# Optimization experiments

Measured on AMD Instinct MI355X. Metric: run time of the kernel, lower is better.

The kernel has to match this reference:

```python
import jax, jax.numpy as jnp
import numpy as np

EPS = 1e-6
SCALE = 1.0
GRID_HEIGHT = 4.0
GRID_RES_Y = 1.0


def _perspective(mat, vec):
    # mat [3,4], vec [...,3] -> (points [...,2], flag [...,3])
    homog = jnp.einsum('ij,...j->...i', mat[:, :3], vec) + mat[:, 3]
    pos = homog[..., 2:3] > 0
    flag = jnp.concatenate([pos, pos, jnp.ones_like(pos)], axis=-1).astype(homog.dtype)
    homog = homog * flag  # zero x,y behind camera; z kept (flag[...,-1]=True)
    return homog[..., :2] / homog[..., 2:3], flag


def _fisheye(pts, k, D, flag):
    cx, cy, fx, fy = k[0, 2], k[1, 2], k[0, 0], k[1, 1]
    x = (pts[..., 0] - cx) / fx
    y = (pts[..., 1] - cy) / fy
    r = jnp.sqrt(x * x + y * y)
    th = jnp.arctan(r)
    t2 = th * th
    rad = th * (1 + D[0] * t2 + D[1] * t2 ** 2 + D[2] * t2 ** 3 + D[5] * t2 ** 4) / r
    xd = x * rad * fx + cx
    yd = y * rad * fy + cy
    return jnp.stack([xd, yd], axis=-1) * flag[..., :2]


def _pinhole(pts, k, D, flag):
    cx, cy, fx, fy = k[0, 2], k[1, 2], k[0, 0], k[1, 1]
    x = (pts[..., 0] - cx) / fx
    y = (pts[..., 1] - cy) / fy
    k1, k2, k3, p1, p2 = D[0], D[1], D[2], D[3], D[4]
    r2 = x * x + y * y
    poly = 1 + k1 * r2 + k2 * r2 * r2 + k3 * r2 * r2 * r2
    xd = x * poly + (2 * p1 * x * y + p2 * (r2 + 2 * x * x))
    yd = y * poly + (p1 * (r2 + 2 * y * y) + 2 * p2 * x * y)
    return jnp.stack([xd * fx + cx, yd * fy + cy], axis=-1) * flag[..., :2]


def _bilinear(img, coords):
    # torch F.grid_sample(align_corners=True, padding_mode='border'); img [C,H,W], coords [...,2] in [-1,1]
    C, H, W = img.shape
    x = jnp.clip((coords[..., 0] + 1) * 0.5 * (W - 1), 0.0, W - 1)
    y = jnp.clip((coords[..., 1] + 1) * 0.5 * (H - 1), 0.0, H - 1)
    x0 = jnp.floor(x)
    y0 = jnp.floor(y)
    wx = x - x0
    wy = y - y0
    x0i = x0.astype(jnp.int32)
    y0i = y0.astype(jnp.int32)
    x1i = jnp.minimum(x0i + 1, W - 1)
    y1i = jnp.minimum(y0i + 1, H - 1)
    flat = img.reshape(C, H * W)

    def g(yi, xi):
        return jnp.take(flat, (yi * W + xi).reshape(-1), axis=1).reshape((C,) + coords.shape[:-1])

    v00 = g(y0i, x0i)
    v01 = g(y0i, x1i)
    v10 = g(y1i, x0i)
    v11 = g(y1i, x1i)
    return v00 * (1 - wx) * (1 - wy) + v01 * wx * (1 - wy) + v10 * (1 - wx) * wy + v11 * wx * wy


def _per_image(feature, k, imu2c, post_rot, post_tran, undist, corner):
    C, Hf, Wf = feature.shape
    calib = k @ imu2c                                  # [3,4]
    pts, flag = _perspective(calib, corner)            # pts [Ny,Zd,Xd,2]
    pts = jnp.where(undist[-1] == 1,
                    _fisheye(pts, k, undist, flag),
                    _pinhole(pts, k, undist, flag))
    pts = jnp.einsum('ij,...j->...i', post_rot[:2, :2], pts) + post_tran[:2]
    nc = jnp.clip(2.0 * (pts / SCALE) - 1.0, -1.0, 1.0)  # [Ny,Zd,Xd,2]
    s0, s1 = slice(None, -1), slice(1, None)
    # 8 voxel corners -> [8, Ny-1, D, Wd, 2]
    corners8 = jnp.stack([nc[a, b, c] for a in (s0, s1) for b in (s0, s1) for c in (s0, s1)], axis=0)
    left = corners8[..., 0].min(0)
    right = corners8[..., 0].max(0)
    top = corners8[..., 1].min(0)
    bot = corners8[..., 1].max(0)
    Nh, D, Wd = left.shape
    bbox = jnp.stack([left, top, right, bot], axis=-1).reshape(Nh, D * Wd, 4)
    area = (bbox[..., 2] - bbox[..., 0]) * (bbox[..., 3] - bbox[..., 1]) * Hf * Wf * 0.25 + EPS  # [Nh,P]
    integ = jnp.cumsum(jnp.cumsum(feature, axis=-1), axis=-2)  # integral image [C,Hf,Wf]
    tl = _bilinear(integ, bbox[..., 0:2])
    br = _bilinear(integ, bbox[..., 2:4])
    tr = _bilinear(integ, jnp.stack([bbox[..., 2], bbox[..., 1]], axis=-1))
    bl = _bilinear(integ, jnp.stack([bbox[..., 0], bbox[..., 3]], axis=-1))
    vox = (tl + br - tr - bl) / area * (area > EPS)    # [C,Nh,P]
    return vox.reshape(C * Nh, D, Wd)                  # neck == '2d'


def _forward(features, ks, imu2cs, post_rots, post_trans, undists, grid):
    ys = -jnp.arange(0.0, GRID_HEIGHT, GRID_RES_Y) + GRID_HEIGHT / 2.0
    y_corners = jnp.stack([jnp.zeros_like(ys), ys, jnp.zeros_like(ys)], axis=-1)  # [Ny,3]
    corners = grid[:, None] + y_corners[None, :, None, None, :]                   # [B,Ny,Zd,Xd,3]
    per_cam = jax.vmap(_per_image, in_axes=(0, 0, 0, 0, 0, 0, None))

    def per_batch(f, k, m, pr, pt, ud, c):
        # drop_idx = [] -> all cameras kept; max over cameras
        return per_cam(f, k, m, pr, pt, ud, c).max(axis=0)

    return jax.vmap(per_batch)(features, ks, imu2cs, post_rots, post_trans, undists, corners)


def setup_inputs():
    key = jax.random.key(0)
    B, N, C, Hf, Wf = 1, 6, 64, 64, 176
    Zd = Xd = 129
    kf, ku = jax.random.split(key, 2)
    features = jax.random.normal(kf, (B, N, C, Hf, Wf), jnp.float32)
    # intrinsics (realistic pinhole values keep the projection numerically sane)
    K = np.zeros((B, N, 3, 3), np.float32)
    K[..., 0, 0] = 600.0
    K[..., 1, 1] = 600.0
    K[..., 0, 2] = 704.0
    K[..., 1, 2] = 256.0
    K[..., 2, 2] = 1.0
    ks = jnp.asarray(K)
    # extrinsics: per-camera yaw + small translation
    m = np.zeros((B, N, 3, 4), np.float32)
    for i in range(N):
        th = 0.25 * (i - 2.5)
        R = np.array([[np.cos(th), 0.0, np.sin(th)],
                      [0.0, 1.0, 0.0],
                      [-np.sin(th), 0.0, np.cos(th)]], np.float32)
        m[:, i, :, :3] = R
        m[:, i, :, 3] = np.array([0.1 * i, -1.5, 0.2], np.float32)
    imu2cs = jnp.asarray(m)
    pr = np.zeros((B, N, 3, 3), np.float32)
    pr[..., 0, 0] = 1.0 / 1408.0
    pr[..., 1, 1] = 1.0 / 512.0
    pr[..., 2, 2] = 1.0
    post_rots = jnp.asarray(pr)
    post_trans = jnp.zeros((B, N, 3), jnp.float32)
    und = 0.01 * np.array(jax.random.normal(ku, (B, N, 7)), np.float32)
    und[..., 6] = 0.0
    und[:, :3, 6] = 1.0  # first 3 cameras fisheye, rest pinhole
    undists = jnp.asarray(und)
    x = np.linspace(-40.0, 40.0, Xd, dtype=np.float32)
    z = np.linspace(3.0, 80.0, Zd, dtype=np.float32)
    zz, xx = np.meshgrid(z, x, indexing='ij')
    g = np.stack([xx, np.zeros_like(xx), zz], axis=-1)[None]  # [1,Zd,Xd,3]
    grid = jnp.asarray(np.broadcast_to(g, (B, Zd, Xd, 3)).copy())
    return {"features": features, "ks": ks, "imu2cs": imu2cs, "post_rots": post_rots,
            "post_trans": post_trans, "undists": undists, "grid": grid}


def reference(features, ks, imu2cs, post_rots, post_trans, undists, grid):
    return _forward(features, ks, imu2cs, post_rots, post_trans, undists, grid)
```

## Files before the change

### kernel.cpp

```cpp
#include <hip/hip_runtime.h>
#include <math.h>

#define NCAM 6
#define C_CH 64
#define HF   64
#define WF   176
#define GDIM 129
#define NY   4
#define NH   3
#define DD   128
#define WDIM 128
#define NP   (DD*WDIM)

#define ROWB (WF*C_CH*4)
#define COLB (C_CH*4)
#define IMGB ((size_t)HF*WF*C_CH*4)


__device__ __forceinline__ float bcf(int x) {
    return __builtin_bit_cast(float, x);
}

__global__ __launch_bounds__(256) void k_rowcum(const float* __restrict__ feat,
                                                float* __restrict__ rowsum)
{
    __shared__ float T[WF * 65];
    __shared__ float S[4][C_CH];
    __shared__ float OFF[4][C_CH];
    const int h   = blockIdx.x;
    const int n   = blockIdx.y;
    const int tid = threadIdx.x;

    for (int idx = tid; idx < C_CH * WF; idx += 256) {
        const int cc = idx / WF;
        const int w  = idx % WF;
        T[w*65 + cc] = feat[((size_t)(n*C_CH + cc)*HF + h)*WF + w];
    }
    __syncthreads();
    {
        const int cc = tid & 63, seg = tid >> 6;
        const int w0 = seg * 44;
        float run = 0.0f;
        #pragma unroll
        for (int i = 0; i < 44; ++i) {
            run += T[(w0 + i)*65 + cc];
            T[(w0 + i)*65 + cc] = run;
        }
        S[seg][cc] = run;
    }
    __syncthreads();
    {
        const int cc = tid & 63, seg = tid >> 6;
        float off = 0.0f;
        #pragma unroll
        for (int s = 0; s < 3; ++s)
            if (s < seg) off += S[s][cc];
        OFF[seg][cc] = off;
    }
    __syncthreads();
    float* outp = rowsum + (size_t)(n*HF + h) * (WF * C_CH);
    for (int idx = tid; idx < WF * C_CH; idx += 256) {
        const int w  = idx >> 6;
        const int cc = idx & 63;
        outp[idx] = T[w*65 + cc] + OFF[w/44][cc];
    }
}

__global__ __launch_bounds__(256) void k_colcum(float* __restrict__ integ)
{
    __shared__ float tA[4][C_CH];
    const int x  = blockIdx.x;
    const int n  = blockIdx.y;
    const int c  = threadIdx.x & 63;
    const int hq = threadIdx.x >> 6;

    float* base = integ + (size_t)n*HF*WF*C_CH + (size_t)x * C_CH + c;
    float e[16];
    #pragma unroll
    for (int i = 0; i < 16; ++i)
        e[i] = base[(size_t)(hq*16 + i) * (WF*C_CH)];
    #pragma unroll
    for (int i = 1; i < 16; ++i)
        e[i] += e[i-1];
    tA[hq][c] = e[15];
    __syncthreads();
    float off = 0.0f;
    #pragma unroll
    for (int s = 0; s < 3; ++s)
        if (s < hq) off += tA[s][c];
    #pragma unroll
    for (int i = 0; i < 16; ++i)
        base[(size_t)(hq*16 + i) * (WF*C_CH)] = e[i] + off;
}

__global__ void k_boxproj(const float* __restrict__ ks,
                          const float* __restrict__ imu2cs,
                          const float* __restrict__ post_rots,
                          const float* __restrict__ post_trans,
                          const float* __restrict__ undists,
                          const float* __restrict__ grid,
                          int4* __restrict__ bp)
{
    const int idx = blockIdx.x * blockDim.x + threadIdx.x;
    if (idx >= NCAM * NH * NP) return;
    const int vox = idx / NCAM;
    const int n   = idx - vox * NCAM;
    const int nh  = vox / NP;
    const int p   = vox - nh * NP;
    const int d   = p / WDIM;
    const int wd  = p - d * WDIM;

    const float* k  = ks         + n * 9;
    const float* m  = imu2cs     + n * 12;
    const float* pr = post_rots  + n * 9;
    const float* pt = post_trans + n * 3;
    const float* D  = undists    + n * 7;

    float cal[12];
    #pragma unroll
    for (int i = 0; i < 3; ++i)
        #pragma unroll
        for (int j = 0; j < 4; ++j)
            cal[i*4+j] = k[i*3+0]*m[0*4+j] + k[i*3+1]*m[1*4+j] + k[i*3+2]*m[2*4+j];

    const float fx = k[0], fy = k[4], cx = k[2], cy = k[5];
    const bool fish = (D[6] == 1.0f);
    const float D0 = D[0], D1 = D[1], D2 = D[2], D3 = D[3], D4 = D[4], D5 = D[5];

    float left = 1e30f, right = -1e30f, top = 1e30f, bot = -1e30f;
    #pragma unroll
    for (int a = 0; a < 2; ++a) {
        const float vy = 2.0f - (float)(nh + a);
        #pragma unroll
        for (int b = 0; b < 2; ++b) {
            #pragma unroll
            for (int cc = 0; cc < 2; ++cc) {
                const int gz = d + b, gx = wd + cc;
                const float vx = grid[(gz*GDIM + gx)*3 + 0];
                const float vz = grid[(gz*GDIM + gx)*3 + 2];

                const float hx = cal[0]*vx + cal[1]*vy + cal[2]*vz  + cal[3];
                const float hy = cal[4]*vx + cal[5]*vy + cal[6]*vz  + cal[7];
                const float hz = cal[8]*vx + cal[9]*vy + cal[10]*vz + cal[11];

                const float fl = (hz > 0.0f) ? 1.0f : 0.0f;
                const float px = (hx * fl) / hz;
                const float py = (hy * fl) / hz;

                const float x = (px - cx) / fx;
                const float y = (py - cy) / fy;

                float xd, yd;
                if (fish) {
                    const float rr = sqrtf(x*x + y*y);
                    const float th = atanf(rr);
                    const float t2 = th * th;
                    const float t4 = t2 * t2;
                    const float rad = th * (1.0f + D0*t2 + D1*t4 + D2*(t2*t4) + D5*(t4*t4)) / rr;
                    xd = x * rad * fx + cx;
                    yd = y * rad * fy + cy;
                } else {
                    const float r2 = x*x + y*y;
                    const float poly = 1.0f + D0*r2 + D1*r2*r2 + D2*r2*r2*r2;
                    const float xdd = x*poly + (2.0f*D3*x*y + D4*(r2 + 2.0f*x*x));
                    const float ydd = y*poly + (D3*(r2 + 2.0f*y*y) + 2.0f*D4*x*y);
                    xd = xdd * fx + cx;
                    yd = ydd * fy + cy;
                }
                xd *= fl; yd *= fl;

                const float qx = pr[0]*xd + pr[1]*yd + pt[0];
                const float qy = pr[3]*xd + pr[4]*yd + pt[1];
                const float ncx = fminf(fmaxf(2.0f*qx - 1.0f, -1.0f), 1.0f);
                const float ncy = fminf(fmaxf(2.0f*qy - 1.0f, -1.0f), 1.0f);

                left  = fminf(left,  ncx);  right = fmaxf(right, ncx);
                top   = fminf(top,   ncy);  bot   = fmaxf(bot,   ncy);
            }
        }
    }

    const float area = (right - left) * (bot - top) * (float)HF * (float)WF * 0.25f + 1e-6f;

    const float xLp = fminf(fmaxf((left  + 1.0f) * 0.5f * (float)(WF-1), 0.0f), (float)(WF-1));
    const float xRp = fminf(fmaxf((right + 1.0f) * 0.5f * (float)(WF-1), 0.0f), (float)(WF-1));
    const float yTp = fminf(fmaxf((top   + 1.0f) * 0.5f * (float)(HF-1), 0.0f), (float)(HF-1));
    const float yBp = fminf(fmaxf((bot   + 1.0f) * 0.5f * (float)(HF-1), 0.0f), (float)(HF-1));
    const float xL0 = floorf(xLp), xR0 = floorf(xRp), yT0 = floorf(yTp), yB0 = floorf(yBp);

    const int pyx = (int)yT0 | ((int)yB0 << 8) | ((int)xL0 << 16) | ((int)xR0 << 24);

    int4 o0, o1;
    o0.x = pyx;
    o0.y = __builtin_bit_cast(int, xLp - xL0);
    o0.z = __builtin_bit_cast(int, xRp - xR0);
    o0.w = __builtin_bit_cast(int, yTp - yT0);
    o1.x = __builtin_bit_cast(int, yBp - yB0);
    o1.y = __builtin_bit_cast(int, area);
    o1.z = 0; o1.w = 0;
    bp[(size_t)idx*2 + 0] = o0;
    bp[(size_t)idx*2 + 1] = o1;
}

__global__ __launch_bounds__(256, 4) void k_sample(const float* __restrict__ integ,
                                                   const int* __restrict__ bpi,
                                                   float* __restrict__ out)
{
    __shared__ float sm[64][65];
    const int nh   = blockIdx.y;
    const int p0   = blockIdx.x * 64;
    const int tid  = threadIdx.x;
    const int wave = __builtin_amdgcn_readfirstlane(tid >> 6);
    const int c    = tid & 63;
    const int pl   = (c < 48) ? c : (c - 48);

    const int* bpw = bpi + (size_t)(nh*NP + p0 + wave*16) * 48;

    int vpc = bpw[pl];
    #pragma unroll 1
    for (int j = 0; j < 16; ++j) {
        int vpn = vpc;
        if (j < 15) vpn = bpw[(j + 1) * 48 + pl];

        float t[6][16];
        float wxl[6], wxr[6], wyt[6], wyb[6], ar[6];
        #pragma unroll
        for (int cam = 0; cam < 6; ++cam) {
            const int f0 = __builtin_amdgcn_readlane(vpc, cam*8 + 0);
            wxl[cam] = bcf(__builtin_amdgcn_readlane(vpc, cam*8 + 1));
            wxr[cam] = bcf(__builtin_amdgcn_readlane(vpc, cam*8 + 2));
            wyt[cam] = bcf(__builtin_amdgcn_readlane(vpc, cam*8 + 3));
            wyb[cam] = bcf(__builtin_amdgcn_readlane(vpc, cam*8 + 4));
            ar[cam]  = bcf(__builtin_amdgcn_readlane(vpc, cam*8 + 5));
            const int yT = f0 & 255, yB = (f0 >> 8) & 255;
            const int xL = (f0 >> 16) & 255, xR = (f0 >> 24) & 255;
            const int r0 = yT * ROWB, r2 = yB * ROWB;
            const int c0 = xL * COLB, c2 = xR * COLB;
            const char* b = (const char*)integ + (size_t)cam * IMGB;
            #pragma unroll
            for (int rr = 0; rr < 4; ++rr) {
                const int ro = ((rr < 2) ? r0 : r2) + ((rr & 1) ? ROWB : 0);
                #pragma unroll
                for (int cc2 = 0; cc2 < 4; ++cc2) {
                    const int co = ((cc2 < 2) ? c0 : c2) + ((cc2 & 1) ? COLB : 0);
                    t[cam][rr*4 + cc2] = ((const float*)(b + (size_t)(ro + co)))[c];
                }
            }
        }

        float vmax = -3.402823466e38f;
        #pragma unroll
        for (int cam = 0; cam < 6; ++cam) {
            const float A0 = fmaf(wxl[cam], t[cam][1]  - t[cam][0],  t[cam][0]);
            const float B0 = fmaf(wxr[cam], t[cam][3]  - t[cam][2],  t[cam][2]);
            const float A1 = fmaf(wxl[cam], t[cam][5]  - t[cam][4],  t[cam][4]);
            const float B1 = fmaf(wxr[cam], t[cam][7]  - t[cam][6],  t[cam][6]);
            const float A2 = fmaf(wxl[cam], t[cam][9]  - t[cam][8],  t[cam][8]);
            const float B2 = fmaf(wxr[cam], t[cam][11] - t[cam][10], t[cam][10]);
            const float A3 = fmaf(wxl[cam], t[cam][13] - t[cam][12], t[cam][12]);
            const float B3 = fmaf(wxr[cam], t[cam][15] - t[cam][14], t[cam][14]);
            const float d0 = A0 - B0, d1 = A1 - B1;
            const float e0 = B2 - A2, e1 = B3 - A3;
            const float s = fmaf(wyt[cam], d1 - d0, d0) + fmaf(wyb[cam], e1 - e0, e0);
            float v = s * __builtin_amdgcn_rcpf(ar[cam]);
            v = (ar[cam] > 1e-6f) ? v : 0.0f;
            vmax = fmaxf(vmax, v);
        }
        sm[wave*16 + j][c] = vmax;
        vpc = vpn;
    }
    __syncthreads();
    #pragma unroll
    for (int it = 0; it < 16; ++it) {
        const int idx = it*256 + tid;
        const int jj = idx & 63;
        const int cc = idx >> 6;
        out[(size_t)(cc*NH + nh)*NP + p0 + jj] = sm[jj][cc];
    }
}

extern "C" void kernel_launch(void* const* d_in, const int* in_sizes, int n_in,
                              void* d_out, int out_size, void* d_ws, size_t ws_size,
                              hipStream_t stream)
{
    const float* feats      = (const float*)d_in[0];
    const float* ks         = (const float*)d_in[1];
    const float* imu2cs     = (const float*)d_in[2];
    const float* post_rots  = (const float*)d_in[3];
    const float* post_trans = (const float*)d_in[4];
    const float* undists    = (const float*)d_in[5];
    const float* grid       = (const float*)d_in[6];
    float* out = (float*)d_out;

    char* ws = (char*)d_ws;
    size_t off = 0;
    float* integ = (float*)(ws + off);
    off += (size_t)NCAM * IMGB + 65536;
    off = (off + 255) & ~(size_t)255;
    int4* bp = (int4*)(ws + off);
    off += (size_t)NCAM * NH * NP * 32 + 256;
    (void)ws_size; (void)in_sizes; (void)n_in; (void)out_size;

    dim3 g1(HF, NCAM);
    k_rowcum<<<g1, 256, 0, stream>>>(feats, integ);

    dim3 g2(WF, NCAM);
    k_colcum<<<g2, 256, 0, stream>>>(integ);

    dim3 g3((NCAM*NH*NP + 255)/256);
    k_boxproj<<<g3, 256, 0, stream>>>(ks, imu2cs, post_rots, post_trans, undists, grid, bp);

    dim3 g4(NP/64, NH);
    k_sample<<<g4, 256, 0, stream>>>(integ, (const int*)bp, out);
}
```

Baseline: 152.1 us.

## Shrink sample tiles, pair cameras to cut registers, add XCD-aware block mapping

The sampling kernel now processes 32 points per block instead of 64 and handles cameras in pairs instead of loading all six cameras' 96 corner values at once. This lowers register pressure so the launch bound can rise to 6 blocks per SIMD. A 1D grid is remapped so consecutive tiles of the same height slice land on the same XCD, which is meant to improve L2 locality of the integral images. The projection kernel swaps IEEE divides for hardware reciprocals, which slightly changes numerics, and pairing cameras exposes less memory-level parallelism per wave.

```diff
diff --git a/kernel.cpp b/kernel.cpp
--- a/kernel.cpp
+++ b/kernel.cpp
@@ -124,6 +124,7 @@
             cal[i*4+j] = k[i*3+0]*m[0*4+j] + k[i*3+1]*m[1*4+j] + k[i*3+2]*m[2*4+j];
 
     const float fx = k[0], fy = k[4], cx = k[2], cy = k[5];
+    const float rfx = 1.0f / fx, rfy = 1.0f / fy;
     const bool fish = (D[6] == 1.0f);
     const float D0 = D[0], D1 = D[1], D2 = D[2], D3 = D[3], D4 = D[4], D5 = D[5];
 
@@ -144,11 +145,12 @@
                 const float hz = cal[8]*vx + cal[9]*vy + cal[10]*vz + cal[11];
 
                 const float fl = (hz > 0.0f) ? 1.0f : 0.0f;
-                const float px = (hx * fl) / hz;
-                const float py = (hy * fl) / hz;
-
-                const float x = (px - cx) / fx;
-                const float y = (py - cy) / fy;
+                const float rhz = __builtin_amdgcn_rcpf(hz);
+                const float px = (hx * fl) * rhz;
+                const float py = (hy * fl) * rhz;
+
+                const float x = (px - cx) * rfx;
+                const float y = (py - cy) * rfy;
 
                 float xd, yd;
                 if (fish) {
@@ -156,7 +158,8 @@
                     const float th = atanf(rr);
                     const float t2 = th * th;
                     const float t4 = t2 * t2;
-                    const float rad = th * (1.0f + D0*t2 + D1*t4 + D2*(t2*t4) + D5*(t4*t4)) / rr;
+                    const float rad = th * (1.0f + D0*t2 + D1*t4 + D2*(t2*t4) + D5*(t4*t4))
+                                      * __builtin_amdgcn_rcpf(rr);
                     xd = x * rad * fx + cx;
                     yd = y * rad * fy + cy;
                 } else {
@@ -202,79 +205,123 @@
     bp[(size_t)idx*2 + 1] = o1;
 }
 
-__global__ __launch_bounds__(256, 4) void k_sample(const float* __restrict__ integ,
+__global__ __launch_bounds__(256, 6) void k_sample(const float* __restrict__ integ,
                                                    const int* __restrict__ bpi,
                                                    float* __restrict__ out)
 {
-    __shared__ float sm[64][65];
-    const int nh   = blockIdx.y;
-    const int p0   = blockIdx.x * 64;
+    __shared__ float sm[32][65];
+    const int bx   = blockIdx.x;
+    const int xcd  = bx & 7;
+    const int slot = bx >> 3;
+    const int gt   = xcd * 192 + slot;
+    const int nh   = gt >> 9;
+    const int p0   = (gt & 511) * 32;
     const int tid  = threadIdx.x;
     const int wave = __builtin_amdgcn_readfirstlane(tid >> 6);
     const int c    = tid & 63;
     const int pl   = (c < 48) ? c : (c - 48);
 
-    const int* bpw = bpi + (size_t)(nh*NP + p0 + wave*16) * 48;
+    const int* bpw = bpi + (size_t)(nh*NP + p0 + wave*8) * 48;
 
     int vpc = bpw[pl];
     #pragma unroll 1
-    for (int j = 0; j < 16; ++j) {
+    for (int j = 0; j < 8; ++j) {
         int vpn = vpc;
-        if (j < 15) vpn = bpw[(j + 1) * 48 + pl];
-
-        float t[6][16];
-        float wxl[6], wxr[6], wyt[6], wyb[6], ar[6];
-        #pragma unroll
-        for (int cam = 0; cam < 6; ++cam) {
-            const int f0 = __builtin_amdgcn_readlane(vpc, cam*8 + 0);
-            wxl[cam] = bcf(__builtin_amdgcn_readlane(vpc, cam*8 + 1));
-            wxr[cam] = bcf(__builtin_amdgcn_readlane(vpc, cam*8 + 2));
-            wyt[cam] = bcf(__builtin_amdgcn_readlane(vpc, cam*8 + 3));
-            wyb[cam] = bcf(__builtin_amdgcn_readlane(vpc, cam*8 + 4));
-            ar[cam]  = bcf(__builtin_amdgcn_readlane(vpc, cam*8 + 5));
-            const int yT = f0 & 255, yB = (f0 >> 8) & 255;
-            const int xL = (f0 >> 16) & 255, xR = (f0 >> 24) & 255;
-            const int r0 = yT * ROWB, r2 = yB * ROWB;
-            const int c0 = xL * COLB, c2 = xR * COLB;
-            const char* b = (const char*)integ + (size_t)cam * IMGB;
-            #pragma unroll
-            for (int rr = 0; rr < 4; ++rr) {
-                const int ro = ((rr < 2) ? r0 : r2) + ((rr & 1) ? ROWB : 0);
+        if (j < 7) vpn = bpw[(j + 1) * 48 + pl];
+
+        float vmax = -3.402823466e38f;
+        #pragma unroll
+        for (int pr2 = 0; pr2 < 3; ++pr2) {
+            const int camA = pr2*2, camB = pr2*2 + 1;
+            const int fA = __builtin_amdgcn_readlane(vpc, camA*8 + 0);
+            const float wxlA = bcf(__builtin_amdgcn_readlane(vpc, camA*8 + 1));
+            const float wxrA = bcf(__builtin_amdgcn_readlane(vpc, camA*8 + 2));
+            const float wytA = bcf(__builtin_amdgcn_readlane(vpc, camA*8 + 3));
+            const float wybA = bcf(__builtin_amdgcn_readlane(vpc, camA*8 + 4));
+            const float arA  = bcf(__builtin_amdgcn_readlane(vpc, camA*8 + 5));
+            const int fB = __builtin_amdgcn_readlane(vpc, camB*8 + 0);
+            const float wxlB = bcf(__builtin_amdgcn_readlane(vpc, camB*8 + 1));
+            const float wxrB = bcf(__builtin_amdgcn_readlane(vpc, camB*8 + 2));
+            const float wytB = bcf(__builtin_amdgcn_readlane(vpc, camB*8 + 3));
+            const float wybB = bcf(__builtin_amdgcn_readlane(vpc, camB*8 + 4));
+            const float arB  = bcf(__builtin_amdgcn_readlane(vpc, camB*8 + 5));
+
+            float tA[16], tB[16];
+            {
+                const int yT = fA & 255, yB2 = (fA >> 8) & 255;
+                const int xL = (fA >> 16) & 255, xR = (fA >> 24) & 255;
+                const int r0 = yT * ROWB, r2 = yB2 * ROWB;
+                const int c0 = xL * COLB, c2 = xR * COLB;
+                const char* b = (const char*)integ + (size_t)camA * IMGB;
                 #pragma unroll
-                for (int cc2 = 0; cc2 < 4; ++cc2) {
-                    const int co = ((cc2 < 2) ? c0 : c2) + ((cc2 & 1) ? COLB : 0);
-                    t[cam][rr*4 + cc2] = ((const float*)(b + (size_t)(ro + co)))[c];
+                for (int rr = 0; rr < 4; ++rr) {
+                    const int ro = ((rr < 2) ? r0 : r2) + ((rr & 1) ? ROWB : 0);
+                    #pragma unroll
+                    for (int cc2 = 0; cc2 < 4; ++cc2) {
+                        const int co = ((cc2 < 2) ? c0 : c2) + ((cc2 & 1) ? COLB : 0);
+                        tA[rr*4 + cc2] = ((const float*)(b + (size_t)(ro + co)))[c];
+                    }
                 }
             }
+            {
+                const int yT = fB & 255, yB2 = (fB >> 8) & 255;
+                const int xL = (fB >> 16) & 255, xR = (fB >> 24) & 255;
+                const int r0 = yT * ROWB, r2 = yB2 * ROWB;
+                const int c0 = xL * COLB, c2 = xR * COLB;
+                const char* b = (const char*)integ + (size_t)camB * IMGB;
+                #pragma unroll
+                for (int rr = 0; rr < 4; ++rr) {
+                    const int ro = ((rr < 2) ? r0 : r2) + ((rr & 1) ? ROWB : 0);
+                    #pragma unroll
+                    for (int cc2 = 0; cc2 < 4; ++cc2) {
+                        const int co = ((cc2 < 2) ? c0 : c2) + ((cc2 & 1) ? COLB : 0);
+                        tB[rr*4 + cc2] = ((const float*)(b + (size_t)(ro + co)))[c];
+                    }
+                }
+            }
+
+            {
+                const float A0 = fmaf(wxlA, tA[1]  - tA[0],  tA[0]);
+                const float B0 = fmaf(wxrA, tA[3]  - tA[2],  tA[2]);
+                const float A1 = fmaf(wxlA, tA[5]  - tA[4],  tA[4]);
+                const float B1 = fmaf(wxrA, tA[7]  - tA[6],  tA[6]);
+                const float A2 = fmaf(wxlA, tA[9]  - tA[8],  tA[8]);
+                const float B2 = fmaf(wxrA, tA[11] - tA[10], tA[10]);
+                const float A3 = fmaf(wxlA, tA[13] - tA[12], tA[12]);
+                const float B3 = fmaf(wxrA, tA[15] - tA[14], tA[14]);
+                const float d0 = A0 - B0, d1 = A1 - B1;
+                const float e0 = B2 - A2, e1 = B3 - A3;
+                const float s = fmaf(wytA, d1 - d0, d0) + fmaf(wybA, e1 - e0, e0);
+                float v = s * __builtin_amdgcn_rcpf(arA);
+                v = (arA > 1e-6f) ? v : 0.0f;
+                vmax = fmaxf(vmax, v);
+            }
+            {
+                const float A0 = fmaf(wxlB, tB[1]  - tB[0],  tB[0]);
+                const float B0 = fmaf(wxrB, tB[3]  - tB[2],  tB[2]);
+                const float A1 = fmaf(wxlB, tB[5]  - tB[4],  tB[4]);
+                const float B1 = fmaf(wxrB, tB[7]  - tB[6],  tB[6]);
+                const float A2 = fmaf(wxlB, tB[9]  - tB[8],  tB[8]);
+                const float B2 = fmaf(wxrB, tB[11] - tB[10], tB[10]);
+                const float A3 = fmaf(wxlB, tB[13] - tB[12], tB[12]);
+                const float B3 = fmaf(wxrB, tB[15] - tB[14], tB[14]);
+                const float d0 = A0 - B0, d1 = A1 - B1;
+                const float e0 = B2 - A2, e1 = B3 - A3;
+                const float s = fmaf(wytB, d1 - d0, d0) + fmaf(wybB, e1 - e0, e0);
+                float v = s * __builtin_amdgcn_rcpf(arB);
+                v = (arB > 1e-6f) ? v : 0.0f;
+                vmax = fmaxf(vmax, v);
+            }
         }
-
-        float vmax = -3.402823466e38f;
-        #pragma unroll
-        for (int cam = 0; cam < 6; ++cam) {
-            const float A0 = fmaf(wxl[cam], t[cam][1]  - t[cam][0],  t[cam][0]);
-            const float B0 = fmaf(wxr[cam], t[cam][3]  - t[cam][2],  t[cam][2]);
-            const float A1 = fmaf(wxl[cam], t[cam][5]  - t[cam][4],  t[cam][4]);
-            const float B1 = fmaf(wxr[cam], t[cam][7]  - t[cam][6],  t[cam][6]);
-            const float A2 = fmaf(wxl[cam], t[cam][9]  - t[cam][8],  t[cam][8]);
-            const float B2 = fmaf(wxr[cam], t[cam][11] - t[cam][10], t[cam][10]);
-            const float A3 = fmaf(wxl[cam], t[cam][13] - t[cam][12], t[cam][12]);
-            const float B3 = fmaf(wxr[cam], t[cam][15] - t[cam][14], t[cam][14]);
-            const float d0 = A0 - B0, d1 = A1 - B1;
-            const float e0 = B2 - A2, e1 = B3 - A3;
-            const float s = fmaf(wyt[cam], d1 - d0, d0) + fmaf(wyb[cam], e1 - e0, e0);
-            float v = s * __builtin_amdgcn_rcpf(ar[cam]);
-            v = (ar[cam] > 1e-6f) ? v : 0.0f;
-            vmax = fmaxf(vmax, v);
-        }
-        sm[wave*16 + j][c] = vmax;
+        sm[wave*8 + j][c] = vmax;
         vpc = vpn;
     }
     __syncthreads();
     #pragma unroll
-    for (int it = 0; it < 16; ++it) {
+    for (int it = 0; it < 8; ++it) {
         const int idx = it*256 + tid;
-        const int jj = idx & 63;
-        const int cc = idx >> 6;
+        const int jj = idx & 31;
+        const int cc = idx >> 5;
         out[(size_t)(cc*NH + nh)*NP + p0 + jj] = sm[jj][cc];
     }
 }
@@ -310,6 +357,6 @@
     dim3 g3((NCAM*NH*NP + 255)/256);
     k_boxproj<<<g3, 256, 0, stream>>>(ks, imu2cs, post_rots, post_trans, undists, grid, bp);
 
-    dim3 g4(NP/64, NH);
+    dim3 g4(NP/32 * NH);
     k_sample<<<g4, 256, 0, stream>>>(integ, (const int*)bp, out);
 }
```

Result: faster. 148.6 us (-2.3%).

## Project grid corners once and vectorize sampling across two voxels per wave

Applied to the files above, without the earlier changes.

Corner projections now run in their own kernel, once per unique grid point per camera, and are stored in a buffer. A separate box-parameter kernel reads them back, replacing the previous eightfold recomputation per voxel. The sampling kernel now has each half-wave handle one voxel with float2 channel loads, uses smaller tiles with an XCD-aware block remap, and raises the occupancy hint. The cost is one more kernel launch, an extra intermediate buffer round-trip through memory, and more register pressure in the sampler.

```diff
diff --git a/kernel.cpp b/kernel.cpp
--- a/kernel.cpp
+++ b/kernel.cpp
@@ -22,7 +22,7 @@
 }
 
 __global__ __launch_bounds__(256) void k_rowcum(const float* __restrict__ feat,
-                                                float* __restrict__ rowsum)
+                                                float* __restrict__ integ)
 {
     __shared__ float T[WF * 65];
     __shared__ float S[4][C_CH];
@@ -58,7 +58,7 @@
         OFF[seg][cc] = off;
     }
     __syncthreads();
-    float* outp = rowsum + (size_t)(n*HF + h) * (WF * C_CH);
+    float* outp = integ + (size_t)(n*HF + h) * (WF * C_CH);
     for (int idx = tid; idx < WF * C_CH; idx += 256) {
         const int w  = idx >> 6;
         const int cc = idx & 63;
@@ -93,13 +93,80 @@
         base[(size_t)(hq*16 + i) * (WF*C_CH)] = e[i] + off;
 }
 
-__global__ void k_boxproj(const float* __restrict__ ks,
+__global__ void k_project(const float* __restrict__ ks,
                           const float* __restrict__ imu2cs,
                           const float* __restrict__ post_rots,
                           const float* __restrict__ post_trans,
                           const float* __restrict__ undists,
                           const float* __restrict__ grid,
-                          int4* __restrict__ bp)
+                          float2* __restrict__ ncbuf)
+{
+    const int n   = blockIdx.y;
+    const int idx = blockIdx.x * blockDim.x + threadIdx.x;
+    const int per = NY * GDIM * GDIM;
+    if (idx >= per) return;
+    const int ny  = idx / (GDIM * GDIM);
+    const int rem = idx % (GDIM * GDIM);
+    const int gz  = rem / GDIM;
+    const int gx  = rem % GDIM;
+
+    const float* k  = ks         + n * 9;
+    const float* m  = imu2cs     + n * 12;
+    const float* pr = post_rots  + n * 9;
+    const float* pt = post_trans + n * 3;
+    const float* D  = undists    + n * 7;
+
+    float cal[12];
+    #pragma unroll
+    for (int i = 0; i < 3; ++i)
+        #pragma unroll
+        for (int j = 0; j < 4; ++j)
+            cal[i*4+j] = k[i*3+0]*m[0*4+j] + k[i*3+1]*m[1*4+j] + k[i*3+2]*m[2*4+j];
+
+    const float vx = grid[(gz*GDIM + gx)*3 + 0];
+    const float vy = 2.0f - (float)ny;
+    const float vz = grid[(gz*GDIM + gx)*3 + 2];
+
+    const float hx = cal[0]*vx + cal[1]*vy + cal[2]*vz  + cal[3];
+    const float hy = cal[4]*vx + cal[5]*vy + cal[6]*vz  + cal[7];
+    const float hz = cal[8]*vx + cal[9]*vy + cal[10]*vz + cal[11];
+
+    const float fl = (hz > 0.0f) ? 1.0f : 0.0f;
+    const float px = (hx * fl) / hz;
+    const float py = (hy * fl) / hz;
+
+    const float fx = k[0], fy = k[4], cx = k[2], cy = k[5];
+    const float x = (px - cx) / fx;
+    const float y = (py - cy) / fy;
+
+    float xd, yd;
+    if (D[6] == 1.0f) {
+        const float r  = sqrtf(x*x + y*y);
+        const float th = atanf(r);
+        const float t2 = th * th;
+        const float t4 = t2 * t2;
+        const float rad = th * (1.0f + D[0]*t2 + D[1]*t4 + D[2]*(t2*t4) + D[5]*(t4*t4)) / r;
+        xd = x * rad * fx + cx;
+        yd = y * rad * fy + cy;
+    } else {
+        const float k1 = D[0], k2 = D[1], k3 = D[2], p1 = D[3], p2 = D[4];
+        const float r2 = x*x + y*y;
+        const float poly = 1.0f + k1*r2 + k2*r2*r2 + k3*r2*r2*r2;
+        const float xdd = x*poly + (2.0f*p1*x*y + p2*(r2 + 2.0f*x*x));
+        const float ydd = y*poly + (p1*(r2 + 2.0f*y*y) + 2.0f*p2*x*y);
+        xd = xdd * fx + cx;
+        yd = ydd * fy + cy;
+    }
+    xd *= fl; yd *= fl;
+
+    const float qx = pr[0]*xd + pr[1]*yd + pt[0];
+    const float qy = pr[3]*xd + pr[4]*yd + pt[1];
+    const float ncx = fminf(fmaxf(2.0f*qx - 1.0f, -1.0f), 1.0f);
+    const float ncy = fminf(fmaxf(2.0f*qy - 1.0f, -1.0f), 1.0f);
+    ncbuf[((n*NY + ny)*GDIM + gz)*GDIM + gx] = make_float2(ncx, ncy);
+}
+
+__global__ void k_boxparams(const float2* __restrict__ ncbuf, int4* __restrict__ bp)
 {
     const int idx = blockIdx.x * blockDim.x + threadIdx.x;
     if (idx >= NCAM * NH * NP) return;
@@ -110,75 +177,17 @@
     const int d   = p / WDIM;
     const int wd  = p - d * WDIM;
 
-    const float* k  = ks         + n * 9;
-    const float* m  = imu2cs     + n * 12;
-    const float* pr = post_rots  + n * 9;
-    const float* pt = post_trans + n * 3;
-    const float* D  = undists    + n * 7;
-
-    float cal[12];
-    #pragma unroll
-    for (int i = 0; i < 3; ++i)
-        #pragma unroll
-        for (int j = 0; j < 4; ++j)
-            cal[i*4+j] = k[i*3+0]*m[0*4+j] + k[i*3+1]*m[1*4+j] + k[i*3+2]*m[2*4+j];
-
-    const float fx = k[0], fy = k[4], cx = k[2], cy = k[5];
-    const bool fish = (D[6] == 1.0f);
-    const float D0 = D[0], D1 = D[1], D2 = D[2], D3 = D[3], D4 = D[4], D5 = D[5];
-
     float left = 1e30f, right = -1e30f, top = 1e30f, bot = -1e30f;
     #pragma unroll
-    for (int a = 0; a < 2; ++a) {
-        const float vy = 2.0f - (float)(nh + a);
-        #pragma unroll
-        for (int b = 0; b < 2; ++b) {
+    for (int a = 0; a < 2; ++a)
+        #pragma unroll
+        for (int b = 0; b < 2; ++b)
             #pragma unroll
             for (int cc = 0; cc < 2; ++cc) {
-                const int gz = d + b, gx = wd + cc;
-                const float vx = grid[(gz*GDIM + gx)*3 + 0];
-                const float vz = grid[(gz*GDIM + gx)*3 + 2];
-
-                const float hx = cal[0]*vx + cal[1]*vy + cal[2]*vz  + cal[3];
-                const float hy = cal[4]*vx + cal[5]*vy + cal[6]*vz  + cal[7];
-                const float hz = cal[8]*vx + cal[9]*vy + cal[10]*vz + cal[11];
-
-                const float fl = (hz > 0.0f) ? 1.0f : 0.0f;
-                const float px = (hx * fl) / hz;
-                const float py = (hy * fl) / hz;
-
-                const float x = (px - cx) / fx;
-                const float y = (py - cy) / fy;
-
-                float xd, yd;
-                if (fish) {
-                    const float rr = sqrtf(x*x + y*y);
-                    const float th = atanf(rr);
-                    const float t2 = th * th;
-                    const float t4 = t2 * t2;
-                    const float rad = th * (1.0f + D0*t2 + D1*t4 + D2*(t2*t4) + D5*(t4*t4)) / rr;
-                    xd = x * rad * fx + cx;
-                    yd = y * rad * fy + cy;
-                } else {
-                    const float r2 = x*x + y*y;
-                    const float poly = 1.0f + D0*r2 + D1*r2*r2 + D2*r2*r2*r2;
-                    const float xdd = x*poly + (2.0f*D3*x*y + D4*(r2 + 2.0f*x*x));
-                    const float ydd = y*poly + (D3*(r2 + 2.0f*y*y) + 2.0f*D4*x*y);
-                    xd = xdd * fx + cx;
-                    yd = ydd * fy + cy;
-                }
-                xd *= fl; yd *= fl;
-
-                const float qx = pr[0]*xd + pr[1]*yd + pt[0];
-                const float qy = pr[3]*xd + pr[4]*yd + pt[1];
-                const float ncx = fminf(fmaxf(2.0f*qx - 1.0f, -1.0f), 1.0f);
-                const float ncy = fminf(fmaxf(2.0f*qy - 1.0f, -1.0f), 1.0f);
-
-                left  = fminf(left,  ncx);  right = fmaxf(right, ncx);
-                top   = fminf(top,   ncy);  bot   = fmaxf(bot,   ncy);
+                const float2 v = ncbuf[((n*NY + nh + a)*GDIM + d + b)*GDIM + wd + cc];
+                left  = fminf(left,  v.x);  right = fmaxf(right, v.x);
+                top   = fminf(top,   v.y);  bot   = fmaxf(bot,   v.y);
             }
-        }
-    }
 
     const float area = (right - left) * (bot - top) * (float)HF * (float)WF * 0.25f + 1e-6f;
 
@@ -202,79 +211,115 @@
     bp[(size_t)idx*2 + 1] = o1;
 }
 
-__global__ __launch_bounds__(256, 4) void k_sample(const float* __restrict__ integ,
+__global__ __launch_bounds__(256, 6) void k_sample(const float* __restrict__ integ,
                                                    const int* __restrict__ bpi,
                                                    float* __restrict__ out)
 {
-    __shared__ float sm[64][65];
-    const int nh   = blockIdx.y;
-    const int p0   = blockIdx.x * 64;
+    __shared__ float sm[32][66];
+    const int bx   = blockIdx.x;
+    const int xcd  = bx & 7;
+    const int slot = bx >> 3;
+    const int gt   = xcd * 192 + slot;
+    const int nh   = gt >> 9;
+    const int p0   = (gt & 511) * 32;
     const int tid  = threadIdx.x;
     const int wave = __builtin_amdgcn_readfirstlane(tid >> 6);
     const int c    = tid & 63;
+    const bool hB  = (c >= 32);
+    const int lch  = c & 31;
     const int pl   = (c < 48) ? c : (c - 48);
 
-    const int* bpw = bpi + (size_t)(nh*NP + p0 + wave*16) * 48;
-
-    int vpc = bpw[pl];
+    const int* bpw = bpi + (size_t)(nh*NP + p0 + wave*8) * 48;
+
+    int vpA = bpw[pl];
+    int vpB = bpw[48 + pl];
     #pragma unroll 1
-    for (int j = 0; j < 16; ++j) {
-        int vpn = vpc;
-        if (j < 15) vpn = bpw[(j + 1) * 48 + pl];
-
-        float t[6][16];
-        float wxl[6], wxr[6], wyt[6], wyb[6], ar[6];
+    for (int i = 0; i < 4; ++i) {
+        int vpA_n = vpA, vpB_n = vpB;
+        if (i < 3) {
+            vpA_n = bpw[(2*i + 2)*48 + pl];
+            vpB_n = bpw[(2*i + 3)*48 + pl];
+        }
+        float vmx = -3.402823466e38f, vmy = -3.402823466e38f;
         #pragma unroll
         for (int cam = 0; cam < 6; ++cam) {
-            const int f0 = __builtin_amdgcn_readlane(vpc, cam*8 + 0);
-            wxl[cam] = bcf(__builtin_amdgcn_readlane(vpc, cam*8 + 1));
-            wxr[cam] = bcf(__builtin_amdgcn_readlane(vpc, cam*8 + 2));
-            wyt[cam] = bcf(__builtin_amdgcn_readlane(vpc, cam*8 + 3));
-            wyb[cam] = bcf(__builtin_amdgcn_readlane(vpc, cam*8 + 4));
-            ar[cam]  = bcf(__builtin_amdgcn_readlane(vpc, cam*8 + 5));
-            const int yT = f0 & 255, yB = (f0 >> 8) & 255;
-            const int xL = (f0 >> 16) & 255, xR = (f0 >> 24) & 255;
-            const int r0 = yT * ROWB, r2 = yB * ROWB;
-            const int c0 = xL * COLB, c2 = xR * COLB;
-            const char* b = (const char*)integ + (size_t)cam * IMGB;
+            const int   fA   = __builtin_amdgcn_readlane(vpA, cam*8 + 0);
+            const float wxlA = bcf(__builtin_amdgcn_readlane(vpA, cam*8 + 1));
+            const float wxrA = bcf(__builtin_amdgcn_readlane(vpA, cam*8 + 2));
+            const float wytA = bcf(__builtin_amdgcn_readlane(vpA, cam*8 + 3));
+            const float wybA = bcf(__builtin_amdgcn_readlane(vpA, cam*8 + 4));
+            const float arA  = bcf(__builtin_amdgcn_readlane(vpA, cam*8 + 5));
+            const int   fB   = __builtin_amdgcn_readlane(vpB, cam*8 + 0);
+            const float wxlB = bcf(__builtin_amdgcn_readlane(vpB, cam*8 + 1));
+            const float wxrB = bcf(__builtin_amdgcn_readlane(vpB, cam*8 + 2));
+            const float wytB = bcf(__builtin_amdgcn_readlane(vpB, cam*8 + 3));
+            const float wybB = bcf(__builtin_amdgcn_readlane(vpB, cam*8 + 4));
+            const float arB  = bcf(__builtin_amdgcn_readlane(vpB, cam*8 + 5));
+
+            const int rTA = (fA & 255) * ROWB,         rBA = ((fA >> 8) & 255) * ROWB;
+            const int cLA = ((fA >> 16) & 255) * COLB, cRA = ((fA >> 24) & 255) * COLB;
+            const int rTB = (fB & 255) * ROWB,         rBB = ((fB >> 8) & 255) * ROWB;
+            const int cLB = ((fB >> 16) & 255) * COLB, cRB = ((fB >> 24) & 255) * COLB;
+
+            const float wxl = hB ? wxlB : wxlA;
+            const float wxr = hB ? wxrB : wxrA;
+            const float wyt = hB ? wytB : wytA;
+            const float wyb = hB ? wybB : wybA;
+            const float ar  = hB ? arB  : arA;
+
+            const char* base = (const char*)integ + (size_t)cam * IMGB + (size_t)(lch * 8);
+            float2 t[16];
             #pragma unroll
-            for (int rr = 0; rr < 4; ++rr) {
-                const int ro = ((rr < 2) ? r0 : r2) + ((rr & 1) ? ROWB : 0);
+            for (int r = 0; r < 4; ++r) {
+                const int roA = ((r < 2) ? rTA : rBA) + ((r & 1) ? ROWB : 0);
+                const int roB = ((r < 2) ? rTB : rBB) + ((r & 1) ? ROWB : 0);
                 #pragma unroll
                 for (int cc2 = 0; cc2 < 4; ++cc2) {
-                    const int co = ((cc2 < 2) ? c0 : c2) + ((cc2 & 1) ? COLB : 0);
-                    t[cam][rr*4 + cc2] = ((const float*)(b + (size_t)(ro + co)))[c];
+                    const int coA = ((cc2 < 2) ? cLA : cRA) + ((cc2 & 1) ? COLB : 0);
+                    const int coB = ((cc2 < 2) ? cLB : cRB) + ((cc2 & 1) ? COLB : 0);
+                    const int off = hB ? (roB + coB) : (roA + coA);
+                    t[r*4 + cc2] = *(const float2*)(base + (size_t)off);
                 }
             }
+
+            const float A0x = fmaf(wxl, t[1].x  - t[0].x,  t[0].x);
+            const float A0y = fmaf(wxl, t[1].y  - t[0].y,  t[0].y);
+            const float B0x = fmaf(wxr, t[3].x  - t[2].x,  t[2].x);
+            const float B0y = fmaf(wxr, t[3].y  - t[2].y,  t[2].y);
+            const float A1x = fmaf(wxl, t[5].x  - t[4].x,  t[4].x);
+            const float A1y = fmaf(wxl, t[5].y  - t[4].y,  t[4].y);
+            const float B1x = fmaf(wxr, t[7].x  - t[6].x,  t[6].x);
+            const float B1y = fmaf(wxr, t[7].y  - t[6].y,  t[6].y);
+            const float A2x = fmaf(wxl, t[9].x  - t[8].x,  t[8].x);
+            const float A2y = fmaf(wxl, t[9].y  - t[8].y,  t[8].y);
+            const float B2x = fmaf(wxr, t[11].x - t[10].x, t[10].x);
+            const float B2y = fmaf(wxr, t[11].y - t[10].y, t[10].y);
+            const float A3x = fmaf(wxl, t[13].x - t[12].x, t[12].x);
+            const float A3y = fmaf(wxl, t[13].y - t[12].y, t[12].y);
+            const float B3x = fmaf(wxr, t[15].x - t[14].x, t[14].x);
+            const float B3y = fmaf(wxr, t[15].y - t[14].y, t[14].y);
+
+            const float d0x = A0x - B0x, d1x = A1x - B1x;
+            const float e0x = B2x - A2x, e1x = B3x - A3x;
+            const float d0y = A0y - B0y, d1y = A1y - B1y;
+            const float e0y = B2y - A2y, e1y = B3y - A3y;
+            const float sx = fmaf(wyt, d1x - d0x, d0x) + fmaf(wyb, e1x - e0x, e0x);
+            const float sy = fmaf(wyt, d1y - d0y, d0y) + fmaf(wyb, e1y - e0y, e0y);
+            const float ia = __builtin_amdgcn_rcpf(ar);
+            const bool ok = (ar > 1e-6f);
+            vmx = fmaxf(vmx, ok ? sx * ia : 0.0f);
+            vmy = fmaxf(vmy, ok ? sy * ia : 0.0f);
         }
-
-        float vmax = -3.402823466e38f;
-        #pragma unroll
-        for (int cam = 0; cam < 6; ++cam) {
-            const float A0 = fmaf(wxl[cam], t[cam][1]  - t[cam][0],  t[cam][0]);
-            const float B0 = fmaf(wxr[cam], t[cam][3]  - t[cam][2],  t[cam][2]);
-            const float A1 = fmaf(wxl[cam], t[cam][5]  - t[cam][4],  t[cam][4]);
-            const float B1 = fmaf(wxr[cam], t[cam][7]  - t[cam][6],  t[cam][6]);
-            const float A2 = fmaf(wxl[cam], t[cam][9]  - t[cam][8],  t[cam][8]);
-            const float B2 = fmaf(wxr[cam], t[cam][11] - t[cam][10], t[cam][10]);
-            const float A3 = fmaf(wxl[cam], t[cam][13] - t[cam][12], t[cam][12]);
-            const float B3 = fmaf(wxr[cam], t[cam][15] - t[cam][14], t[cam][14]);
-            const float d0 = A0 - B0, d1 = A1 - B1;
-            const float e0 = B2 - A2, e1 = B3 - A3;
-            const float s = fmaf(wyt[cam], d1 - d0, d0) + fmaf(wyb[cam], e1 - e0, e0);
-            float v = s * __builtin_amdgcn_rcpf(ar[cam]);
-            v = (ar[cam] > 1e-6f) ? v : 0.0f;
-            vmax = fmaxf(vmax, v);
-        }
-        sm[wave*16 + j][c] = vmax;
-        vpc = vpn;
-    }
-    __syncthreads();
-    #pragma unroll
-    for (int it = 0; it < 16; ++it) {
+        const int vox = wave*8 + 2*i + (hB ? 1 : 0);
+        *(float2*)&sm[vox][2*lch] = make_float2(vmx, vmy);
+        vpA = vpA_n; vpB = vpB_n;
+    }
+    __syncthreads();
+    #pragma unroll
+    for (int it = 0; it < 8; ++it) {
         const int idx = it*256 + tid;
-        const int jj = idx & 63;
-        const int cc = idx >> 6;
+        const int jj = idx & 31;
+        const int cc = idx >> 5;
         out[(size_t)(cc*NH + nh)*NP + p0 + jj] = sm[jj][cc];
     }
 }
@@ -295,7 +340,10 @@
     char* ws = (char*)d_ws;
     size_t off = 0;
     float* integ = (float*)(ws + off);
-    off += (size_t)NCAM * IMGB + 65536;
+    off += (size_t)NCAM * IMGB + ROWB + 65536;
+    off = (off + 255) & ~(size_t)255;
+    float2* ncbuf = (float2*)(ws + off);
+    off += sizeof(float2) * (size_t)NCAM * NY * GDIM * GDIM;
     off = (off + 255) & ~(size_t)255;
     int4* bp = (int4*)(ws + off);
     off += (size_t)NCAM * NH * NP * 32 + 256;
@@ -307,9 +355,12 @@
     dim3 g2(WF, NCAM);
     k_colcum<<<g2, 256, 0, stream>>>(integ);
 
-    dim3 g3((NCAM*NH*NP + 255)/256);
-    k_boxproj<<<g3, 256, 0, stream>>>(ks, imu2cs, post_rots, post_trans, undists, grid, bp);
-
-    dim3 g4(NP/64, NH);
-    k_sample<<<g4, 256, 0, stream>>>(integ, (const int*)bp, out);
-}
+    dim3 g3((NY*GDIM*GDIM + 255)/256, NCAM);
+    k_project<<<g3, 256, 0, stream>>>(ks, imu2cs, post_rots, post_trans, undists, grid, ncbuf);
+
+    dim3 g4((NCAM*NH*NP + 255)/256);
+    k_boxparams<<<g4, 256, 0, stream>>>(ncbuf, bp);
+
+    dim3 g5(NP/32 * NH);
+    k_sample<<<g5, 256, 0, stream>>>(integ, (const int*)bp, out);
+}
```

Measured after the change: 172.0 us. 13.1% more time.
